# Performance work log

Measured on AMD Instinct MI355X. Metric: run time of the kernel, lower is better.

## Reference

```python
import jax, jax.numpy as jnp
import numpy as np

MAX_DISTANCE = 9          # search radius (pixels, at half resolution)
PAD_VAL = 1e10            # padding value; sigmoid saturates to 1 exactly as with 1e20,
                          # but avoids inf in fp32 squared sums (same output, safe grads)


def _offsets(m):
    k = 2 * m + 1
    offs = np.stack(np.meshgrid(np.arange(k), np.arange(k), indexing='ij'), -1)
    return jnp.asarray(offs.reshape(-1, 2))  # [K,2], row-major (dy, dx) like torch unfold


def _interp_matrix(out_size, in_size):
    # 1-D bilinear interpolation matrix, align_corners=True (matches F.interpolate)
    scale = (in_size - 1) / (out_size - 1)
    pos = jnp.arange(out_size, dtype=jnp.float32) * scale
    lo = jnp.clip(jnp.floor(pos).astype(jnp.int32), 0, in_size - 2)
    frac = pos - lo.astype(jnp.float32)
    rows = jnp.arange(out_size)
    M = jnp.zeros((out_size, in_size), jnp.float32)
    return M.at[rows, lo].add(1.0 - frac).at[rows, lo + 1].add(frac)


def _local_distances(query, prev, m):
    # local_pairwise_distances2 with MODEL_LOCAL_DOWNSAMPLE=True
    H, W, C = query.shape
    x = query.reshape(H // 2, 2, W // 2, 2, C).mean(axis=(1, 3))  # avg_pool2d 2x2
    y = prev.reshape(H // 2, 2, W // 2, 2, C).mean(axis=(1, 3))
    h, w = H // 2, W // 2
    ypad = jnp.pad(y, ((m, m), (m, m), (0, 0)), constant_values=PAD_VAL)
    offs = _offsets(m)

    def one(off):
        sl = jax.lax.dynamic_slice(ypad, (off[0], off[1], 0), (h, w, C))
        return jnp.sum((x - sl) ** 2, axis=-1)  # [h,w]

    d = jax.vmap(one)(offs)                      # [K,h,w]
    d = (jax.nn.sigmoid(d) - 0.5) * 2.0
    d = jnp.transpose(d, (1, 2, 0))              # [h,w,K]
    Mh = _interp_matrix(H, h)
    Mw = _interp_matrix(W, w)
    return jnp.einsum('Hh,Ww,hwk->HWk', Mh, Mw, d)  # bilinear upsample


def setup_inputs() -> dict:
    key = jax.random.key(0)
    k1, k2, k3 = jax.random.split(key, 3)
    H, W, C, n_objs = 96, 160, 100, 3
    return {
        'prev_frame_embedding': jax.random.normal(k1, (H, W, C), jnp.float32),
        'query_embedding': jax.random.normal(k2, (H, W, C), jnp.float32),
        'prev_frame_labels': jax.random.randint(k3, (H, W, 1), 0, n_objs).astype(jnp.int32),
        'gt_ids': jnp.arange(n_objs, dtype=jnp.int32),
    }


def reference(prev_frame_embedding, query_embedding, prev_frame_labels, gt_ids):
    m = MAX_DISTANCE
    H, W, _ = prev_frame_embedding.shape
    n = gt_ids.shape[0]
    d = _local_distances(query_embedding, prev_frame_embedding, m)  # [H,W,K]

    masks = prev_frame_labels == gt_ids[None, None, :]  # [H,W,n] bool
    mpad = jnp.pad(masks, ((m, m), (m, m), (0, 0)))      # pad False
    offs = _offsets(m)

    def one(off):
        return jax.lax.dynamic_slice(mpad, (off[0], off[1], 0), (H, W, n))

    om = jnp.transpose(jax.vmap(one)(offs), (1, 2, 0, 3))  # [H,W,K,n]
    d_masked = jnp.where(om, d[..., None], 1.0)
    dists = jnp.min(d_masked, axis=2)                      # [H,W,n]
    return dists.reshape(1, H, W, n, 1)
```

## Files before the change

kernel.cpp:

```cpp
#include <hip/hip_runtime.h>
#include <hip/hip_bf16.h>
#include <math.h>

#define HF 96
#define WF 160
#define CH 100
#define HH 48
#define HW 80
#define NPIX 3840
#define MD 9
#define KD 19
#define K2 361
#define NMAX 8

#define OFF_XT 0
#define OFF_YT (CH*NPIX)
#define OFF_XS (2*CH*NPIX)
#define OFF_YS (2*CH*NPIX + NPIX)
#define OFF_DH (2*CH*NPIX + 2*NPIX)

typedef float f32x2 __attribute__((ext_vector_type(2)));

__global__ __launch_bounds__(256) void pool_kernel(
    const float* __restrict__ q, const float* __restrict__ p,
    float* __restrict__ Xt, float* __restrict__ Yt,
    float* __restrict__ xs, float* __restrict__ ys) {
  int w = threadIdx.x >> 6, L = threadIdx.x & 63;
  int pix = blockIdx.x * 4 + w;
  int i = pix / HW, j = pix - i * HW;
  int base = (2 * i) * WF * CH + (2 * j) * CH;
  float nx = 0.f, ny = 0.f;
  for (int c = L; c < CH; c += 64) {
    int b = base + c;
    float xv = 0.25f * (q[b] + q[b + CH] + q[b + WF * CH] + q[b + WF * CH + CH]);
    float yv = 0.25f * (p[b] + p[b + CH] + p[b + WF * CH] + p[b + WF * CH + CH]);
    Xt[c * NPIX + pix] = xv;
    Yt[c * NPIX + pix] = yv;
    nx = fmaf(xv, xv, nx);
    ny = fmaf(yv, yv, ny);
  }
  for (int s = 32; s > 0; s >>= 1) {
    nx += __shfl_down(nx, s);
    ny += __shfl_down(ny, s);
  }
  if (L == 0) { xs[pix] = nx; ys[pix] = ny; }
}

__global__ __launch_bounds__(256, 3) void dist_kernel(
    const float* __restrict__ Xt, const float* __restrict__ Yt,
    const float* __restrict__ xs, const float* __restrict__ ys,
    __hip_bfloat16* __restrict__ dh2) {
  __shared__ float ex[3][64][41];
  int il = threadIdx.x & 63;
  int qtr = threadIdx.x >> 6;
  int item = blockIdx.x * 64 + il;
  int t = item % 960, u = item / 960;
  int dp = u >> 1, h = u & 1;
  int ipq = t / HW, j = t - ipq * HW;
  int pix0 = ipq * (4 * HW) + j;
  int r = 4 * ipq + dp - MD;
  bool rowOK = (r >= 0 && r < HH);
  int cbase = j - MD + 10 * h;
  int nd = h ? 9 : 10;

  f32x2 accA[10], accB[10];
#pragma unroll
  for (int d = 0; d < 10; ++d) { accA[d] = (f32x2){0.f, 0.f}; accB[d] = (f32x2){0.f, 0.f}; }

  if (rowOK) {
    const float* xp = Xt + (qtr * 25) * NPIX + pix0;
    const float* yp = Yt + (qtr * 25) * NPIX + r * HW + cbase;
#pragma unroll 5
    for (int c = 0; c < 25; ++c) {
      float x0 = xp[0], x1 = xp[HW], x2 = xp[2 * HW], x3 = xp[3 * HW];
      f32x2 xA = {x0, x1}, xB = {x2, x3};
#pragma unroll
      for (int d = 0; d < 10; ++d) {
        float yv = yp[d];
        f32x2 yy = {yv, yv};
        accA[d] = __builtin_elementwise_fma(xA, yy, accA[d]);
        accB[d] = __builtin_elementwise_fma(xB, yy, accB[d]);
      }
      xp += NPIX; yp += NPIX;
    }
  }

  if (qtr > 0 && rowOK) {
#pragma unroll
    for (int d = 0; d < 10; ++d) {
      ex[qtr - 1][il][4 * d + 0] = accA[d].x;
      ex[qtr - 1][il][4 * d + 1] = accA[d].y;
      ex[qtr - 1][il][4 * d + 2] = accB[d].x;
      ex[qtr - 1][il][4 * d + 3] = accB[d].y;
    }
  }
  __syncthreads();
  if (qtr != 0) return;

  if (!rowOK) {
    __hip_bfloat16 one = __float2bfloat16(1.0f);
#pragma unroll
    for (int rr = 0; rr < 4; ++rr) {
      int dy = dp - rr;
      if (dy < 0 || dy >= KD) continue;
      int kb = dy * KD + 10 * h;
      int pix = pix0 + rr * HW;
#pragma unroll
      for (int d = 0; d < 10; ++d) {
        if (d >= nd) break;
        dh2[(kb + d) * NPIX + pix] = one;
      }
    }
    return;
  }

#pragma unroll
  for (int q = 0; q < 3; ++q)
#pragma unroll
    for (int d = 0; d < 10; ++d) {
      accA[d].x += ex[q][il][4 * d + 0];
      accA[d].y += ex[q][il][4 * d + 1];
      accB[d].x += ex[q][il][4 * d + 2];
      accB[d].y += ex[q][il][4 * d + 3];
    }

  const float* ysr = ys + r * HW;
  float yss[10];
  bool okc[10];
#pragma unroll
  for (int d = 0; d < 10; ++d) {
    int jj = cbase + d;
    okc[d] = (jj >= 0) && (jj < HW);
    int jcl = jj < 0 ? 0 : (jj > HW - 1 ? HW - 1 : jj);
    yss[d] = ysr[jcl];
  }

#pragma unroll
  for (int rr = 0; rr < 4; ++rr) {
    int dy = dp - rr;
    if (dy < 0 || dy >= KD) continue;
    int kb = dy * KD + 10 * h;
    int pix = pix0 + rr * HW;
    float xss = xs[pix];
#pragma unroll
    for (int d = 0; d < 10; ++d) {
      if (d >= nd) break;
      float a = (rr == 0) ? accA[d].x : (rr == 1) ? accA[d].y
              : (rr == 2) ? accB[d].x : accB[d].y;
      float s = xss + yss[d] - 2.f * a;
      float e = __expf(-s);
      float rv = okc[d] ? (1.f - e) / (1.f + e) : 1.0f;
      dh2[(kb + d) * NPIX + pix] = __float2bfloat16(rv);
    }
  }
}

template <int N>
__global__ __launch_bounds__(1024) void upmin_kernel(
    const __hip_bfloat16* __restrict__ dh2, const int* __restrict__ labels,
    const int* __restrict__ gt, float* __restrict__ out) {
  int w = threadIdx.x >> 6;
  int lane = threadIdx.x & 63;
  int pixel = blockIdx.x * 64 + lane;
  int I = pixel / WF, J = pixel - I * WF;

  const float sy = (float)((HH - 1.0) / (HF - 1.0));
  const float sx = (float)((HW - 1.0) / (WF - 1.0));
  float py = (float)I * sy;
  int y0 = (int)floorf(py); if (y0 > HH - 2) y0 = HH - 2; if (y0 < 0) y0 = 0;
  float fy = py - (float)y0;
  float px = (float)J * sx;
  int x0 = (int)floorf(px); if (x0 > HW - 2) x0 = HW - 2; if (x0 < 0) x0 = 0;
  float fx = px - (float)x0;
  float w00 = (1.f - fy) * (1.f - fx), w01 = (1.f - fy) * fx;
  float w10 = fy * (1.f - fx),         w11 = fy * fx;
  int np00 = y0 * HW + x0;

  int gtl[N];
  float mins[N];
#pragma unroll
  for (int o = 0; o < N; ++o) { gtl[o] = gt[o]; mins[o] = 1.0f; }

  for (int k = w; k < K2; k += 16) {
    int dy = k / KD, dx = k - dy * KD;
    int P = I + dy - MD, Q = J + dx - MD;
    const __hip_bfloat16* dk = dh2 + k * NPIX + np00;
    float v = w00 * __bfloat162float(dk[0]) + w01 * __bfloat162float(dk[1]) +
              w10 * __bfloat162float(dk[HW]) + w11 * __bfloat162float(dk[HW + 1]);
    if (P >= 0 && P < HF && Q >= 0 && Q < WF) {
      int lab = labels[P * WF + Q];
#pragma unroll
      for (int o = 0; o < N; ++o)
        if (lab == gtl[o]) mins[o] = fminf(mins[o], v);
    }
  }

  __shared__ float mm[16][64][N];
#pragma unroll
  for (int o = 0; o < N; ++o) mm[w][lane][o] = mins[o];
  __syncthreads();
  if (w < 8) {
#pragma unroll
    for (int o = 0; o < N; ++o)
      mm[w][lane][o] = fminf(mm[w][lane][o], mm[w + 8][lane][o]);
  }
  __syncthreads();
  if (w < 4) {
#pragma unroll
    for (int o = 0; o < N; ++o)
      mm[w][lane][o] = fminf(mm[w][lane][o], mm[w + 4][lane][o]);
  }
  __syncthreads();
  if (w == 0) {
#pragma unroll
    for (int o = 0; o < N; ++o) {
      float m = fminf(fminf(mm[0][lane][o], mm[1][lane][o]),
                      fminf(mm[2][lane][o], mm[3][lane][o]));
      out[pixel * N + o] = m;
    }
  }
}

extern "C" void kernel_launch(void* const* d_in, const int* in_sizes, int n_in,
                              void* d_out, int out_size, void* d_ws, size_t ws_size,
                              hipStream_t stream) {
  const float* prev  = (const float*)d_in[0];
  const float* query = (const float*)d_in[1];
  const int* labels  = (const int*)d_in[2];
  const int* gt      = (const int*)d_in[3];
  int n = in_sizes[3];
  if (n > NMAX) n = NMAX;
  float* ws = (float*)d_ws;
  float* Xt = ws + OFF_XT;
  float* Yt = ws + OFF_YT;
  float* xs = ws + OFF_XS;
  float* ys = ws + OFF_YS;
  __hip_bfloat16* dh2 = (__hip_bfloat16*)(ws + OFF_DH);
  float* out = (float*)d_out;

  hipLaunchKernelGGL(pool_kernel, dim3(NPIX / 4), dim3(256), 0, stream,
                     query, prev, Xt, Yt, xs, ys);
  hipLaunchKernelGGL(dist_kernel, dim3(660), dim3(256), 0, stream,
                     Xt, Yt, xs, ys, dh2);
  dim3 ug(HF * WF / 64), ub(1024);
  switch (n) {
    case 1: hipLaunchKernelGGL(upmin_kernel<1>, ug, ub, 0, stream, dh2, labels, gt, out); break;
    case 2: hipLaunchKernelGGL(upmin_kernel<2>, ug, ub, 0, stream, dh2, labels, gt, out); break;
    case 3: hipLaunchKernelGGL(upmin_kernel<3>, ug, ub, 0, stream, dh2, labels, gt, out); break;
    case 4: hipLaunchKernelGGL(upmin_kernel<4>, ug, ub, 0, stream, dh2, labels, gt, out); break;
    case 5: hipLaunchKernelGGL(upmin_kernel<5>, ug, ub, 0, stream, dh2, labels, gt, out); break;
    case 6: hipLaunchKernelGGL(upmin_kernel<6>, ug, ub, 0, stream, dh2, labels, gt, out); break;
    case 7: hipLaunchKernelGGL(upmin_kernel<7>, ug, ub, 0, stream, dh2, labels, gt, out); break;
    default: hipLaunchKernelGGL(upmin_kernel<8>, ug, ub, 0, stream, dh2, labels, gt, out); break;
  }
}
```

Baseline: 104.7 us.

## Stage Y rows in per-wave LDS double buffer and pack bf16 pair loads

In dist_kernel, each wavefront cooperatively loads the two Y rows its 64 items need as 16-byte vectors into a per-wave LDS buffer. The buffer is double-buffered across channels, so the inner FMA loop reads Y from LDS instead of issuing scattered global loads. It relies on lockstep execution within a wave instead of a barrier, and adds LDS traffic plus clamped, possibly out-of-range reads that are masked later. In upmin_kernel, the two horizontally adjacent bf16 values are fetched with one 32-bit load and unpacked with shifts and masks instead of four separate bf16 conversions.

```diff
diff --git a/kernel.cpp b/kernel.cpp
--- a/kernel.cpp
+++ b/kernel.cpp
@@ -20,6 +20,7 @@
 #define OFF_DH (2*CH*NPIX + 2*NPIX)
 
 typedef float f32x2 __attribute__((ext_vector_type(2)));
+typedef float f32x4 __attribute__((ext_vector_type(4)));
 
 __global__ __launch_bounds__(256) void pool_kernel(
     const float* __restrict__ q, const float* __restrict__ p,
@@ -51,6 +52,7 @@
     const float* __restrict__ xs, const float* __restrict__ ys,
     __hip_bfloat16* __restrict__ dh2) {
   __shared__ float ex[3][64][41];
+  __shared__ __align__(16) float ybuf[4][2][212];
   int il = threadIdx.x & 63;
   int qtr = threadIdx.x >> 6;
   int item = blockIdx.x * 64 + il;
@@ -63,25 +65,48 @@
   int cbase = j - MD + 10 * h;
   int nd = h ? 9 : 10;
 
+  int tbase = (blockIdx.x * 64) % 960;
+  int ip0 = tbase / HW;
+  int g = ipq - ip0;
+  int r0 = 4 * ip0 + dp - MD;
+  int rc0 = r0 < 0 ? 0 : (r0 > HH - 1 ? HH - 1 : r0);
+  int r1 = r0 + 4;
+  int rc1 = r1 < 0 ? 0 : (r1 > HH - 1 ? HH - 1 : r1);
+
   f32x2 accA[10], accB[10];
 #pragma unroll
   for (int d = 0; d < 10; ++d) { accA[d] = (f32x2){0.f, 0.f}; accB[d] = (f32x2){0.f, 0.f}; }
 
-  if (rowOK) {
+  if (__any(rowOK)) {
+    int sg = il / 26, chunk = il - sg * 26;
+    const float* sp = Yt + (qtr * 25) * NPIX + (sg ? rc1 : rc0) * HW + (4 * chunk - 12);
     const float* xp = Xt + (qtr * 25) * NPIX + pix0;
-    const float* yp = Yt + (qtr * 25) * NPIX + r * HW + cbase;
+    int lbase = g * 104 + j + 10 * h + 3;
+    f32x4 sreg;
+    if (il < 52) {
+      sreg = *(const f32x4*)sp;
+      *(f32x4*)&ybuf[qtr][0][sg * 104 + 4 * chunk] = sreg;
+      sp += NPIX;
+      sreg = *(const f32x4*)sp;
+    }
 #pragma unroll 5
     for (int c = 0; c < 25; ++c) {
       float x0 = xp[0], x1 = xp[HW], x2 = xp[2 * HW], x3 = xp[3 * HW];
+      xp += NPIX;
       f32x2 xA = {x0, x1}, xB = {x2, x3};
+      const float* yb = &ybuf[qtr][c & 1][0];
 #pragma unroll
       for (int d = 0; d < 10; ++d) {
-        float yv = yp[d];
+        float yv = yb[lbase + d];
         f32x2 yy = {yv, yv};
         accA[d] = __builtin_elementwise_fma(xA, yy, accA[d]);
         accB[d] = __builtin_elementwise_fma(xB, yy, accB[d]);
       }
-      xp += NPIX; yp += NPIX;
+      if (il < 52) {
+        *(f32x4*)&ybuf[qtr][(c + 1) & 1][sg * 104 + 4 * chunk] = sreg;
+        sp += NPIX;
+        sreg = *(const f32x4*)sp;
+      }
     }
   }
 
@@ -185,8 +210,14 @@
     int dy = k / KD, dx = k - dy * KD;
     int P = I + dy - MD, Q = J + dx - MD;
     const __hip_bfloat16* dk = dh2 + k * NPIX + np00;
-    float v = w00 * __bfloat162float(dk[0]) + w01 * __bfloat162float(dk[1]) +
-              w10 * __bfloat162float(dk[HW]) + w11 * __bfloat162float(dk[HW + 1]);
+    unsigned int u01, u23;
+    __builtin_memcpy(&u01, dk, 4);
+    __builtin_memcpy(&u23, dk + HW, 4);
+    float f00 = __uint_as_float(u01 << 16);
+    float f01 = __uint_as_float(u01 & 0xffff0000u);
+    float f10 = __uint_as_float(u23 << 16);
+    float f11 = __uint_as_float(u23 & 0xffff0000u);
+    float v = w00 * f00 + w01 * f01 + w10 * f10 + w11 * f11;
     if (P >= 0 && P < HF && Q >= 0 && Q < WF) {
       int lab = labels[P * WF + Q];
 #pragma unroll
```

Result: no change. 104.0 us (-0.7%).
